# Kernel tuning notes

Hardware: AMD Instinct MI355X
Metric: run time of the kernel (lower is better)

## Reference

```python
import jax, jax.numpy as jnp
import numpy as np

T, B, F, H, L = 512, 64, 128, 512, 3
SCALES = [1, 2, 4]  # 2**l for l in range(n_layers)


def setup_inputs() -> dict:
    key = jax.random.key(0)
    ks = jax.random.split(key, 10)
    s = 0.05
    inp = {"inputs": jax.random.normal(ks[0], (B, T, F), jnp.float32)}
    in_dims = [F, H, H]
    i = 1
    for l in range(L):
        inp[f"wi{l}"] = jax.random.normal(ks[i], (in_dims[l], H), jnp.float32) * s; i += 1
        inp[f"ws{l}"] = jax.random.normal(ks[i], (F, H), jnp.float32) * s; i += 1
        inp[f"wh{l}"] = jax.random.normal(ks[i], (H, H), jnp.float32) * s; i += 1
    return inp


def _scaled(x, scale):
    # x: [T, B, F]; moving average over time with window `scale`, stride 1
    if scale == 1:
        return x
    cs = jnp.concatenate([jnp.zeros((1,) + x.shape[1:], x.dtype), jnp.cumsum(x, axis=0)], axis=0)
    return (cs[scale:] - cs[:-scale]) / scale  # [T-scale+1, B, F]


def _layer(inp, sx, wi, ws, wh, scale):
    # loop i in range(len(sx) - scale), index = scale-1+i; hidden starts at zeros
    n = sx.shape[0] - scale
    xs = inp[scale - 1:scale - 1 + n]   # [n, B, din]
    sxs = sx[scale - 1:scale - 1 + n]   # [n, B, F]
    h0 = jnp.zeros((inp.shape[1], wh.shape[0]), inp.dtype)

    def step(h, xt):
        x_t, s_t = xt
        h = jnp.tanh(x_t @ wi + h @ wh + s_t @ ws)
        return h, h

    _, out = jax.lax.scan(step, h0, (xs, sxs))
    return out  # [n, B, H]


def reference(inputs, wi0, ws0, wh0, wi1, ws1, wh1, wi2, ws2, wh2):
    x = jnp.transpose(inputs, (1, 0, 2))  # batch_first -> [T, B, F]
    weights = [(wi0, ws0, wh0), (wi1, ws1, wh1), (wi2, ws2, wh2)]
    outs = []
    cur = x
    for l, scale in enumerate(SCALES):
        sx = _scaled(x, scale)  # scaled input always from original sequence
        cur = _layer(cur, sx, *weights[l], scale)
        outs.append(cur)
    return tuple(outs)
```

## Files before the change

kernel.cpp:

```cpp
#include <hip/hip_runtime.h>

#define T_DIM 512
#define B_DIM 64
#define F_DIM 128
#define H_DIM 512

typedef _Float16 f16x8 __attribute__((ext_vector_type(8)));
typedef _Float16 f16x4 __attribute__((ext_vector_type(4)));
typedef float f32x4 __attribute__((ext_vector_type(4)));

__global__ void prepT(_Float16* __restrict__ dst, const float* __restrict__ src) {
  int idx = blockIdx.x * blockDim.x + threadIdx.x;
  if (idx < 262144) {
    int j = idx >> 9, k = idx & 511;
    dst[idx] = (_Float16)src[k * 512 + j];
  }
}

__global__ void prep_wcat2(_Float16* __restrict__ dst, const float* __restrict__ wi0,
                           const float* __restrict__ ws0, const float* __restrict__ ws1,
                           const float* __restrict__ ws2) {
  const long total = 3L * 512 * 640;
  for (long idx = (long)blockIdx.x * blockDim.x + threadIdx.x; idx < total;
       idx += (long)gridDim.x * blockDim.x) {
    int l = (int)(idx / 327680);
    int rem = (int)(idx % 327680);
    int n = rem / 640, kc = rem % 640;
    float v = 0.f;
    if (l == 0) {
      if (kc < 128) v = wi0[kc * 512 + n];
      else if (kc < 256) v = ws0[(kc - 128) * 512 + n];
    } else {
      const float* ws = (l == 1) ? ws1 : ws2;
      if (kc < 128) v = ws[kc * 512 + n];
    }
    dst[idx] = (_Float16)v;
  }
}

__global__ void build_A(_Float16* __restrict__ Abuf, const float* __restrict__ xin,
                        const float* __restrict__ prev, int n, int inK, int scale,
                        int layer) {
  const int Kcat = inK + 128;
  const long total = (long)n * 64 * Kcat;
  for (long idx = (long)blockIdx.x * blockDim.x + threadIdx.x; idx < total;
       idx += (long)gridDim.x * blockDim.x) {
    int k = (int)(idx % Kcat);
    long r = idx / Kcat;
    int b = (int)(r & 63);
    int t = (int)(r >> 6);
    float v;
    if (k < inK) {
      if (layer == 0) v = xin[((long)b * T_DIM + t) * F_DIM + k];
      else v = prev[((long)(t + scale - 1) * B_DIM + b) * H_DIM + k];
    } else {
      int kk = k - inK;
      int t0 = t + scale - 1;
      float s = 0.f;
      for (int w = 0; w < scale; ++w) s += xin[((long)b * T_DIM + t0 + w) * F_DIM + kk];
      v = s * (1.f / scale);
    }
    Abuf[idx] = (_Float16)v;
  }
}

__global__ __launch_bounds__(256) void gemm_f16(const _Float16* __restrict__ A,
                                                const _Float16* __restrict__ Bt,
                                                float* __restrict__ C, int Mrows,
                                                int Kcat) {
  __shared__ _Float16 As[128][72];
  __shared__ _Float16 Bs[128][72];
  const int tid = threadIdx.x;
  const int tn = blockIdx.x, tm = blockIdx.y;
  const int lane = tid & 63, wid = tid >> 6;
  const int wm = wid >> 1, wn = wid & 1;
  f32x4 acc[4][4] = {};
  const int nK = Kcat >> 6;
  const int lrow = tid >> 3, lkc = (tid & 7) * 8;

  for (int kt = 0; kt < nK; ++kt) {
    for (int r = 0; r < 4; ++r) {
      int row = r * 32 + lrow;
      int grow = tm * 128 + row;
      uint4 va = make_uint4(0u, 0u, 0u, 0u);
      if (grow < Mrows) va = *(const uint4*)&A[(size_t)grow * Kcat + kt * 64 + lkc];
      *(uint4*)&As[row][lkc] = va;
      uint4 vb = *(const uint4*)&Bt[(size_t)(tn * 128 + row) * 640 + kt * 64 + lkc];
      *(uint4*)&Bs[row][lkc] = vb;
    }
    __syncthreads();
#pragma unroll
    for (int kk = 0; kk < 64; kk += 32) {
      f16x8 af[4], bf[4];
#pragma unroll
      for (int mt = 0; mt < 4; ++mt)
        af[mt] = *(const f16x8*)&As[wm * 64 + mt * 16 + (lane & 15)][kk + (lane >> 4) * 8];
#pragma unroll
      for (int nt = 0; nt < 4; ++nt)
        bf[nt] = *(const f16x8*)&Bs[wn * 64 + nt * 16 + (lane & 15)][kk + (lane >> 4) * 8];
#pragma unroll
      for (int mt = 0; mt < 4; ++mt)
#pragma unroll
        for (int nt = 0; nt < 4; ++nt)
          acc[mt][nt] = __builtin_amdgcn_mfma_f32_16x16x32_f16(af[mt], bf[nt], acc[mt][nt], 0, 0, 0);
    }
    __syncthreads();
  }

  const int crow0 = tm * 128 + wm * 64 + (lane >> 4) * 4;
  const int ccol0 = tn * 128 + wn * 64 + (lane & 15);
#pragma unroll
  for (int mt = 0; mt < 4; ++mt)
#pragma unroll
    for (int q = 0; q < 4; ++q) {
      int grow = crow0 + mt * 16 + q;
      if (grow < Mrows) {
#pragma unroll
        for (int nt = 0; nt < 4; ++nt)
          C[(size_t)grow * 512 + ccol0 + nt * 16] = acc[mt][nt][q];
      }
    }
}

__global__ void zero_cnt(int* __restrict__ c, int ntot) {
  int i = blockIdx.x * blockDim.x + threadIdx.x;
  if (i < ntot) c[i] = 0;
}

__global__ __launch_bounds__(512, 2) void pipeline(
    float* __restrict__ out, const _Float16* __restrict__ whT16,
    const _Float16* __restrict__ wiT16, int* __restrict__ prog) {
  __shared__ _Float16 stageBuf[2][16 * 512];
  __shared__ _Float16 Blds[4 * 32 * 64 * 8];

  const int wg = blockIdx.x;
  const int s = wg >> 2, g = wg & 2 ? (wg & 3) : (wg & 3);
  const int gg = wg & 3;
  (void)s; (void)g;
  const int stage = wg >> 2;
  const int tid = threadIdx.x;
  const int lane = tid & 63, wid = tid >> 6;
  const int colbase = wid * 64;
  const int bq = lane & 15;
  const int u = lane >> 4;
  const int gnb = wid * 4;

  const int nL[3] = {511, 509, 505};
  const size_t offL[3] = {0, 511ul * 32768, (511ul + 509ul) * 32768};

  if ((stage == 0) || (stage == 3) || (stage == 6)) {
    const int l = stage / 3;
    const int n = nL[l];
    float* po = out + offL[l];
    const _Float16* whT = whT16 + (size_t)l * 262144;
    int* pub = (l < 2) ? prog + stage * 4 + gg : nullptr;
    const int* src = (l > 0) ? prog + (stage - 1) * 4 + gg : nullptr;
    const int b0g = gg * 16;

    {
      uint4* B4 = (uint4*)Blds;
      for (int p = 0; p < 16; ++p) {
        int flat = p * 512 + tid;
        int ll = flat & 63;
        int gn = (flat >> 6) & 31;
        int kbl = flat >> 11;
        B4[flat] = *(const uint4*)&whT[(size_t)(gn * 16 + (ll & 15)) * 512 +
                                       (kbl + 10) * 32 + (ll >> 4) * 8];
      }
    }
    f16x8 bfr[4][10];
    {
#pragma unroll
      for (int nt = 0; nt < 4; ++nt) {
        const int j = colbase + nt * 16 + bq;
#pragma unroll
        for (int kb = 0; kb < 10; ++kb)
          bfr[nt][kb] = *(const f16x8*)&whT[(size_t)j * 512 + kb * 32 + u * 8];
      }
#pragma unroll
      for (int nt = 0; nt < 4; ++nt)
#pragma unroll
        for (int kb = 0; kb < 10; ++kb) asm volatile("" : "+v"(bfr[nt][kb]));
    }
    __syncthreads();

    const size_t base = (size_t)(b0g + bq) * 512 + colbase + u * 4;

#define AFRD(kb) (*(const f16x8*)&hs[((kb)*64 + u * 16 + (bq ^ (u & 1))) * 8])
#define BLRD(kb, nt) \
  (*(const f16x8*)&Blds[((((kb)-10) * 32 + gnb + (nt)) * 64 + lane) * 8])
#define GLOAD(kb, nt) \
  (*(const f16x8*)&whT[(size_t)(colbase + (nt)*16 + bq) * 512 + (kb)*32 + u * 8])

    for (int t = 0; t < n; ++t) {
      if (src && (t & 7) == 0) {
        if (tid == 0) {
          int target = t + 8 < n ? t + 8 : n;
          long it = 0;
          while (__hip_atomic_load(src, __ATOMIC_ACQUIRE, __HIP_MEMORY_SCOPE_AGENT) < target)
            if (++it > 100000000L) break;
        }
        __syncthreads();
        __threadfence();
      }

      const float* pc = po + (size_t)t * 32768 + base;
      f32x4 pre[4];
#pragma unroll
      for (int nt = 0; nt < 4; ++nt) pre[nt] = *(const f32x4*)&pc[nt * 16];

      f32x4 acc[4] = {};
      if (t > 0) {
        const _Float16* hs = stageBuf[(t - 1) & 1];
        constexpr int seq[16] = {10, 0, 1, 2, 3, 11, 4, 5, 14, 12, 6, 7, 13, 8, 9, 15};
        constexpr int lnx[16] = {11, -1, -1, -1, -1, 12, -1, -1, -1, 13, -1, -1, -1, -1, -1, -1};
        f16x8 afr[4];
#pragma unroll
        for (int i = 0; i < 4; ++i) afr[i] = AFRD(seq[i]);
        f16x8 blr[4];
#pragma unroll
        for (int nt = 0; nt < 4; ++nt) blr[nt] = BLRD(10, nt);
        f16x8 gfr[4];
#pragma unroll
        for (int nt = 0; nt < 4; ++nt) gfr[nt] = GLOAD(14, nt);

#pragma unroll
        for (int i = 0; i < 16; ++i) {
          const int kb = seq[i];
          f16x8 a = afr[i & 3];
          if (i + 4 < 16) afr[i & 3] = AFRD(seq[i + 4]);
          if (kb < 10) {
#pragma unroll
            for (int nt = 0; nt < 4; ++nt)
              acc[nt] = __builtin_amdgcn_mfma_f32_16x16x32_f16(bfr[nt][kb], a, acc[nt], 0, 0, 0);
          } else if (kb < 14) {
            f16x8 w[4];
#pragma unroll
            for (int nt = 0; nt < 4; ++nt) w[nt] = blr[nt];
            if (lnx[i] >= 0) {
#pragma unroll
              for (int nt = 0; nt < 4; ++nt) blr[nt] = BLRD(lnx[i], nt);
            }
#pragma unroll
            for (int nt = 0; nt < 4; ++nt)
              acc[nt] = __builtin_amdgcn_mfma_f32_16x16x32_f16(w[nt], a, acc[nt], 0, 0, 0);
          } else if (kb == 14) {
            f16x8 w[4];
#pragma unroll
            for (int nt = 0; nt < 4; ++nt) w[nt] = gfr[nt];
#pragma unroll
            for (int nt = 0; nt < 4; ++nt) gfr[nt] = GLOAD(15, nt);
#pragma unroll
            for (int nt = 0; nt < 4; ++nt)
              acc[nt] = __builtin_amdgcn_mfma_f32_16x16x32_f16(w[nt], a, acc[nt], 0, 0, 0);
          } else {
#pragma unroll
            for (int nt = 0; nt < 4; ++nt)
              acc[nt] = __builtin_amdgcn_mfma_f32_16x16x32_f16(gfr[nt], a, acc[nt], 0, 0, 0);
          }
        }
      }

      _Float16* hw = stageBuf[t & 1];
      float* pw = po + (size_t)t * 32768 + base;
#pragma unroll
      for (int nt = 0; nt < 4; ++nt) {
        const int J = colbase + nt * 16 + u * 4;
        const int slot = (J >> 5) * 64 + ((J >> 3) & 3) * 16 + (bq ^ ((J >> 3) & 1));
        f16x4 h4;
#pragma unroll
        for (int q = 0; q < 4; ++q) {
          float a = acc[nt][q] + pre[nt][q];
          float e = __builtin_amdgcn_exp2f(a * 2.8853900817779268f);
          float h = 1.f - 2.f * __builtin_amdgcn_rcpf(e + 1.f);
          acc[nt][q] = h;
          h4[q] = (_Float16)h;
        }
        *(f16x4*)&hw[slot * 8 + (J & 7)] = h4;
        *(f32x4*)&pw[nt * 16] = acc[nt];
      }

      if (pub && (((t & 7) == 7) || (t == n - 1))) {
        asm volatile("s_waitcnt vmcnt(0) lgkmcnt(0)\n\ts_barrier" ::: "memory");
        __threadfence();
        if (tid == 0)
          __hip_atomic_store(pub, t + 1, __ATOMIC_RELEASE, __HIP_MEMORY_SCOPE_AGENT);
      } else {
        asm volatile("s_waitcnt lgkmcnt(0)\n\ts_barrier" ::: "memory");
      }
    }
#undef AFRD
#undef BLRD
#undef GLOAD
  } else {
    const int l = (stage <= 2) ? 1 : 2;
    const int ha = (stage == 2 || stage == 5) ? 1 : 0;
    const int n = nL[l], nprev = nL[l - 1];
    const int off = (l == 1) ? 1 : 3;
    const float* xsrc = out + offL[l - 1];
    float* pdst = out + offL[l];
    const _Float16* wiT = wiT16 + (size_t)(l - 1) * 262144;
    int* pub = prog + stage * 4 + gg;
    const int* srcX = prog + ((l == 1) ? 0 : 3) * 4 + gg;
    const int* srcA = ha ? (prog + (stage - 1) * 4 + gg) : nullptr;

    f16x8 bfr8[4][8];
    {
#pragma unroll
      for (int nt = 0; nt < 4; ++nt) {
        const int j = colbase + nt * 16 + bq;
#pragma unroll
        for (int kb = 0; kb < 8; ++kb)
          bfr8[nt][kb] = *(const f16x8*)&wiT[(size_t)j * 512 + (ha * 8 + kb) * 32 + u * 8];
      }
#pragma unroll
      for (int nt = 0; nt < 4; ++nt)
#pragma unroll
        for (int kb = 0; kb < 8; ++kb) asm volatile("" : "+v"(bfr8[nt][kb]));
    }

    const int bx = tid & 15;
    const int jbi = tid >> 4;
    const int slotW = (jbi >> 2) * 64 + (jbi & 3) * 16 + (bx ^ (jbi & 1));
    const size_t xrowbase = (size_t)(gg * 16 + bx) * 512 + ha * 256 + jbi * 8;
    const size_t base = (size_t)(gg * 16 + bq) * 512 + colbase + u * 4;

    if (tid == 0) {
      int target = 9 + off < nprev ? 9 + off : nprev;
      long it = 0;
      while (__hip_atomic_load(srcX, __ATOMIC_ACQUIRE, __HIP_MEMORY_SCOPE_AGENT) < target)
        if (++it > 100000000L) break;
      if (srcA) {
        int ta = 8 < n ? 8 : n;
        it = 0;
        while (__hip_atomic_load(srcA, __ATOMIC_ACQUIRE, __HIP_MEMORY_SCOPE_AGENT) < ta)
          if (++it > 100000000L) break;
      }
    }
    __syncthreads();
    __threadfence();
    {
      const float* xr = xsrc + (size_t)off * 32768 + xrowbase;
      float4 xa = *(const float4*)&xr[0];
      float4 xb = *(const float4*)&xr[4];
      f16x8 xh;
      xh[0] = (_Float16)xa.x; xh[1] = (_Float16)xa.y;
      xh[2] = (_Float16)xa.z; xh[3] = (_Float16)xa.w;
      xh[4] = (_Float16)xb.x; xh[5] = (_Float16)xb.y;
      xh[6] = (_Float16)xb.z; xh[7] = (_Float16)xb.w;
      *(f16x8*)&stageBuf[0][slotW * 8] = xh;
    }
    asm volatile("s_waitcnt lgkmcnt(0)\n\ts_barrier" ::: "memory");

#define AFP(kb) \
  (*(const f16x8*)&hs[((kb)*64 + u * 16 + (bq ^ (u & 1))) * 8])

    for (int t = 0; t < n; ++t) {
      if ((t & 7) == 0 && t) {
        if (tid == 0) {
          int target = t + 9 + off < nprev ? t + 9 + off : nprev;
          long it = 0;
          while (__hip_atomic_load(srcX, __ATOMIC_ACQUIRE, __HIP_MEMORY_SCOPE_AGENT) < target)
            if (++it > 100000000L) break;
          if (srcA) {
            int ta = t + 8 < n ? t + 8 : n;
            it = 0;
            while (__hip_atomic_load(srcA, __ATOMIC_ACQUIRE, __HIP_MEMORY_SCOPE_AGENT) < ta)
              if (++it > 100000000L) break;
          }
        }
        __syncthreads();
        __threadfence();
      }

      const bool havN = (t + 1 < n);
      float4 xa, xb;
      if (havN) {
        const float* xr = xsrc + (size_t)(t + 1 + off) * 32768 + xrowbase;
        xa = *(const float4*)&xr[0];
        xb = *(const float4*)&xr[4];
      }

      f32x4 acc[4] = {};
      {
        const _Float16* hs = stageBuf[t & 1];
        f16x8 afr[4];
#pragma unroll
        for (int i = 0; i < 4; ++i) afr[i] = AFP(i);
#pragma unroll
        for (int kb = 0; kb < 8; ++kb) {
          f16x8 a = afr[kb & 3];
          if (kb < 4) afr[kb & 3] = AFP(kb + 4);
#pragma unroll
          for (int nt = 0; nt < 4; ++nt)
            acc[nt] = __builtin_amdgcn_mfma_f32_16x16x32_f16(bfr8[nt][kb], a, acc[nt], 0, 0, 0);
        }
      }

      float* pw = pdst + (size_t)t * 32768 + base;
#pragma unroll
      for (int nt = 0; nt < 4; ++nt) {
        f32x4 v = *(const f32x4*)&pw[nt * 16];
        v += acc[nt];
        *(f32x4*)&pw[nt * 16] = v;
      }

      if (havN) {
        f16x8 xh;
        xh[0] = (_Float16)xa.x; xh[1] = (_Float16)xa.y;
        xh[2] = (_Float16)xa.z; xh[3] = (_Float16)xa.w;
        xh[4] = (_Float16)xb.x; xh[5] = (_Float16)xb.y;
        xh[6] = (_Float16)xb.z; xh[7] = (_Float16)xb.w;
        *(f16x8*)&stageBuf[(t + 1) & 1][slotW * 8] = xh;
      }

      if (((t & 7) == 7) || (t == n - 1)) {
        asm volatile("s_waitcnt vmcnt(0) lgkmcnt(0)\n\ts_barrier" ::: "memory");
        __threadfence();
        if (tid == 0)
          __hip_atomic_store(pub, t + 1, __ATOMIC_RELEASE, __HIP_MEMORY_SCOPE_AGENT);
      } else {
        asm volatile("s_waitcnt lgkmcnt(0)\n\ts_barrier" ::: "memory");
      }
    }
#undef AFP
  }
}

extern "C" void kernel_launch(void* const* d_in, const int* in_sizes, int n_in,
                              void* d_out, int out_size, void* d_ws, size_t ws_size,
                              hipStream_t stream) {
  const float* inputs = (const float*)d_in[0];
  const float* wi[3] = {(const float*)d_in[1], (const float*)d_in[4], (const float*)d_in[7]};
  const float* wsm[3] = {(const float*)d_in[2], (const float*)d_in[5], (const float*)d_in[8]};
  const float* wh[3] = {(const float*)d_in[3], (const float*)d_in[6], (const float*)d_in[9]};
  float* out = (float*)d_out;

  char* wsp = (char*)d_ws;
  _Float16* whT16 = (_Float16*)wsp;
  _Float16* wiT16 = (_Float16*)(wsp + 1572864);
  _Float16* wcat = (_Float16*)(wsp + 2621440);
  int* prog = (int*)(wsp + 4587520);
  _Float16* Abuf = (_Float16*)(wsp + 4587776);

  zero_cnt<<<1, 64, 0, stream>>>(prog, 24);
  for (int l = 0; l < 3; ++l)
    prepT<<<1024, 256, 0, stream>>>(whT16 + (size_t)l * 262144, wh[l]);
  prepT<<<1024, 256, 0, stream>>>(wiT16, wi[1]);
  prepT<<<1024, 256, 0, stream>>>(wiT16 + 262144, wi[2]);
  prep_wcat2<<<1024, 256, 0, stream>>>(wcat, wi[0], wsm[0], wsm[1], wsm[2]);

  const int nL[3] = {511, 509, 505};
  const long offL[3] = {0L, 511L * 32768, (511L + 509L) * 32768};

  build_A<<<4096, 256, 0, stream>>>(Abuf, inputs, nullptr, nL[0], 128, 1, 0);
  gemm_f16<<<dim3(4, (nL[0] * 64 + 127) / 128), 256, 0, stream>>>(
      Abuf, wcat, out, nL[0] * 64, 256);
  build_A<<<2048, 256, 0, stream>>>(Abuf, inputs, nullptr, nL[1], 0, 2, 1);
  gemm_f16<<<dim3(4, (nL[1] * 64 + 127) / 128), 256, 0, stream>>>(
      Abuf, wcat + 512 * 640, out + offL[1], nL[1] * 64, 128);
  build_A<<<2048, 256, 0, stream>>>(Abuf, inputs, nullptr, nL[2], 0, 4, 1);
  gemm_f16<<<dim3(4, (nL[2] * 64 + 127) / 128), 256, 0, stream>>>(
      Abuf, wcat + 2 * 512 * 640, out + offL[2], nL[2] * 64, 128);

  pipeline<<<28, 512, 0, stream>>>(out, whT16, wiT16, prog);
}
```

Measured before the change: 2.964 ms.

## Restructure pipeline into 5 stages with fp16 ring buffers between layers

Reduces the persistent pipeline from 7 stages (28 workgroups) to 5 stages (20 workgroups). Each input-projection stage now runs a full K=512 MFMA per timestep instead of two K=256 half-stages. Hidden states go between stages through 64-entry fp16 ring buffers, and input projections are passed as fp16 values to the next recurrent stage. That stage adds them before tanh, which replaces the fp32 read-modify-write of the output. Back-pressure counters with a 40-step lag keep the rings from overflowing, at the cost of extra spin-waits and fp16 rounding of the projected inputs.

New measurement: 3.239 ms. 1.09x slower.

```diff
diff --git a/kernel.cpp b/kernel.cpp
--- a/kernel.cpp
+++ b/kernel.cpp
@@ -129,15 +129,14 @@
 
 __global__ __launch_bounds__(512, 2) void pipeline(
     float* __restrict__ out, const _Float16* __restrict__ whT16,
-    const _Float16* __restrict__ wiT16, int* __restrict__ prog) {
+    const _Float16* __restrict__ wiT16, _Float16* __restrict__ h16r,
+    _Float16* __restrict__ preIr, int* __restrict__ prog) {
   __shared__ _Float16 stageBuf[2][16 * 512];
   __shared__ _Float16 Blds[4 * 32 * 64 * 8];
 
   const int wg = blockIdx.x;
-  const int s = wg >> 2, g = wg & 2 ? (wg & 3) : (wg & 3);
+  const int stage = wg >> 2;
   const int gg = wg & 3;
-  (void)s; (void)g;
-  const int stage = wg >> 2;
   const int tid = threadIdx.x;
   const int lane = tid & 63, wid = tid >> 6;
   const int colbase = wid * 64;
@@ -147,121 +146,139 @@
 
   const int nL[3] = {511, 509, 505};
   const size_t offL[3] = {0, 511ul * 32768, (511ul + 509ul) * 32768};
-
-  if ((stage == 0) || (stage == 3) || (stage == 6)) {
-    const int l = stage / 3;
-    const int n = nL[l];
-    float* po = out + offL[l];
-    const _Float16* whT = whT16 + (size_t)l * 262144;
-    int* pub = (l < 2) ? prog + stage * 4 + gg : nullptr;
-    const int* src = (l > 0) ? prog + (stage - 1) * 4 + gg : nullptr;
-    const int b0g = gg * 16;
-
-    {
-      uint4* B4 = (uint4*)Blds;
-      for (int p = 0; p < 16; ++p) {
-        int flat = p * 512 + tid;
-        int ll = flat & 63;
-        int gn = (flat >> 6) & 31;
-        int kbl = flat >> 11;
-        B4[flat] = *(const uint4*)&whT[(size_t)(gn * 16 + (ll & 15)) * 512 +
-                                       (kbl + 10) * 32 + (ll >> 4) * 8];
-      }
-    }
-    f16x8 bfr[4][10];
-    {
-#pragma unroll
-      for (int nt = 0; nt < 4; ++nt) {
-        const int j = colbase + nt * 16 + bq;
-#pragma unroll
-        for (int kb = 0; kb < 10; ++kb)
-          bfr[nt][kb] = *(const f16x8*)&whT[(size_t)j * 512 + kb * 32 + u * 8];
-      }
-#pragma unroll
-      for (int nt = 0; nt < 4; ++nt)
-#pragma unroll
-        for (int kb = 0; kb < 10; ++kb) asm volatile("" : "+v"(bfr[nt][kb]));
-    }
-    __syncthreads();
-
-    const size_t base = (size_t)(b0g + bq) * 512 + colbase + u * 4;
+  const bool isRec = (stage & 1) == 0;
+  const int l = isRec ? (stage >> 1) : ((stage + 1) >> 1);
+
+  const _Float16* W = isRec ? (whT16 + (size_t)l * 262144)
+                            : (wiT16 + (size_t)(l - 1) * 262144);
+
+  {
+    uint4* B4 = (uint4*)Blds;
+    for (int p = 0; p < 16; ++p) {
+      int flat = p * 512 + tid;
+      int ll = flat & 63;
+      int gn = (flat >> 6) & 31;
+      int kbl = flat >> 11;
+      B4[flat] = *(const uint4*)&W[(size_t)(gn * 16 + (ll & 15)) * 512 +
+                                   (kbl + 10) * 32 + (ll >> 4) * 8];
+    }
+  }
+  f16x8 bfr[4][10];
+  {
+#pragma unroll
+    for (int nt = 0; nt < 4; ++nt) {
+      const int j = colbase + nt * 16 + bq;
+#pragma unroll
+      for (int kb = 0; kb < 10; ++kb)
+        bfr[nt][kb] = *(const f16x8*)&W[(size_t)j * 512 + kb * 32 + u * 8];
+    }
+#pragma unroll
+    for (int nt = 0; nt < 4; ++nt)
+#pragma unroll
+      for (int kb = 0; kb < 10; ++kb) asm volatile("" : "+v"(bfr[nt][kb]));
+  }
+  __syncthreads();
 
 #define AFRD(kb) (*(const f16x8*)&hs[((kb)*64 + u * 16 + (bq ^ (u & 1))) * 8])
 #define BLRD(kb, nt) \
   (*(const f16x8*)&Blds[((((kb)-10) * 32 + gnb + (nt)) * 64 + lane) * 8])
 #define GLOAD(kb, nt) \
-  (*(const f16x8*)&whT[(size_t)(colbase + (nt)*16 + bq) * 512 + (kb)*32 + u * 8])
+  (*(const f16x8*)&W[(size_t)(colbase + (nt)*16 + bq) * 512 + (kb)*32 + u * 8])
+
+#define MFMA16()                                                                 \
+  {                                                                              \
+    constexpr int seq[16] = {10, 0, 1, 2, 3, 11, 4, 5, 14, 12, 6, 7, 13, 8, 9, 15}; \
+    constexpr int lnx[16] = {11, -1, -1, -1, -1, 12, -1, -1, -1, 13, -1, -1, -1, -1, -1, -1}; \
+    f16x8 afr[4];                                                                \
+    _Pragma("unroll") for (int i = 0; i < 4; ++i) afr[i] = AFRD(seq[i]);         \
+    f16x8 blr[4];                                                                \
+    _Pragma("unroll") for (int nt = 0; nt < 4; ++nt) blr[nt] = BLRD(10, nt);     \
+    f16x8 gfr[4];                                                                \
+    _Pragma("unroll") for (int nt = 0; nt < 4; ++nt) gfr[nt] = GLOAD(14, nt);    \
+    _Pragma("unroll") for (int i = 0; i < 16; ++i) {                             \
+      const int kb = seq[i];                                                     \
+      f16x8 a = afr[i & 3];                                                      \
+      if (i + 4 < 16) afr[i & 3] = AFRD(seq[i + 4]);                             \
+      if (kb < 10) {                                                             \
+        _Pragma("unroll") for (int nt = 0; nt < 4; ++nt)                         \
+            acc[nt] = __builtin_amdgcn_mfma_f32_16x16x32_f16(bfr[nt][kb], a,     \
+                                                             acc[nt], 0, 0, 0); \
+      } else if (kb < 14) {                                                      \
+        f16x8 w[4];                                                              \
+        _Pragma("unroll") for (int nt = 0; nt < 4; ++nt) w[nt] = blr[nt];        \
+        if (lnx[i] >= 0) {                                                       \
+          _Pragma("unroll") for (int nt = 0; nt < 4; ++nt) blr[nt] =             \
+              BLRD(lnx[i], nt);                                                  \
+        }                                                                        \
+        _Pragma("unroll") for (int nt = 0; nt < 4; ++nt)                         \
+            acc[nt] = __builtin_amdgcn_mfma_f32_16x16x32_f16(w[nt], a, acc[nt],  \
+                                                             0, 0, 0);          \
+      } else if (kb == 14) {                                                     \
+        f16x8 w[4];                                                              \
+        _Pragma("unroll") for (int nt = 0; nt < 4; ++nt) w[nt] = gfr[nt];        \
+        _Pragma("unroll") for (int nt = 0; nt < 4; ++nt) gfr[nt] = GLOAD(15, nt);\
+        _Pragma("unroll") for (int nt = 0; nt < 4; ++nt)                         \
+            acc[nt] = __builtin_amdgcn_mfma_f32_16x16x32_f16(w[nt], a, acc[nt],  \
+                                                             0, 0, 0);          \
+      } else {                                                                   \
+        _Pragma("unroll") for (int nt = 0; nt < 4; ++nt)                         \
+            acc[nt] = __builtin_amdgcn_mfma_f32_16x16x32_f16(gfr[nt], a,         \
+                                                             acc[nt], 0, 0, 0); \
+      }                                                                          \
+    }                                                                            \
+  }
+
+  if (isRec) {
+    const int n = nL[l];
+    float* po = out + offL[l];
+    int* pub = prog + stage * 4 + gg;
+    const int* fwd = (l > 0) ? prog + (stage - 1) * 4 + gg : nullptr;
+    const int* bpc = (l < 2) ? prog + (stage + 1) * 4 + gg : nullptr;
+    const _Float16* preIrd =
+        (l > 0) ? preIr + ((size_t)(l - 1) * 4 + gg) * 524288 : nullptr;
+    _Float16* h16w = (l < 2) ? h16r + ((size_t)l * 4 + gg) * 524288 : nullptr;
+    const int b0g = gg * 16;
+    const size_t base = (size_t)(b0g + bq) * 512 + colbase + u * 4;
+    const int riOff = bq * 512 + colbase + u * 4;
 
     for (int t = 0; t < n; ++t) {
-      if (src && (t & 7) == 0) {
+      if ((t & 7) == 0) {
         if (tid == 0) {
-          int target = t + 8 < n ? t + 8 : n;
           long it = 0;
-          while (__hip_atomic_load(src, __ATOMIC_ACQUIRE, __HIP_MEMORY_SCOPE_AGENT) < target)
-            if (++it > 100000000L) break;
+          if (fwd) {
+            int tgt = t + 8 < n ? t + 8 : n;
+            while (__hip_atomic_load(fwd, __ATOMIC_ACQUIRE, __HIP_MEMORY_SCOPE_AGENT) < tgt)
+              if (++it > 200000000L) break;
+          }
+          if (bpc && t > 40) {
+            it = 0;
+            while (__hip_atomic_load(bpc, __ATOMIC_ACQUIRE, __HIP_MEMORY_SCOPE_AGENT) < t - 40)
+              if (++it > 200000000L) break;
+          }
         }
         __syncthreads();
         __threadfence();
       }
 
       const float* pc = po + (size_t)t * 32768 + base;
-      f32x4 pre[4];
-#pragma unroll
-      for (int nt = 0; nt < 4; ++nt) pre[nt] = *(const f32x4*)&pc[nt * 16];
+      f32x4 preS[4];
+#pragma unroll
+      for (int nt = 0; nt < 4; ++nt) preS[nt] = *(const f32x4*)&pc[nt * 16];
+      f16x4 pi4[4];
+      if (preIrd) {
+        const _Float16* ps = preIrd + (size_t)(t & 63) * 8192 + riOff;
+#pragma unroll
+        for (int nt = 0; nt < 4; ++nt) pi4[nt] = *(const f16x4*)&ps[nt * 16];
+      }
 
       f32x4 acc[4] = {};
       if (t > 0) {
         const _Float16* hs = stageBuf[(t - 1) & 1];
-        constexpr int seq[16] = {10, 0, 1, 2, 3, 11, 4, 5, 14, 12, 6, 7, 13, 8, 9, 15};
-        constexpr int lnx[16] = {11, -1, -1, -1, -1, 12, -1, -1, -1, 13, -1, -1, -1, -1, -1, -1};
-        f16x8 afr[4];
-#pragma unroll
-        for (int i = 0; i < 4; ++i) afr[i] = AFRD(seq[i]);
-        f16x8 blr[4];
-#pragma unroll
-        for (int nt = 0; nt < 4; ++nt) blr[nt] = BLRD(10, nt);
-        f16x8 gfr[4];
-#pragma unroll
-        for (int nt = 0; nt < 4; ++nt) gfr[nt] = GLOAD(14, nt);
-
-#pragma unroll
-        for (int i = 0; i < 16; ++i) {
-          const int kb = seq[i];
-          f16x8 a = afr[i & 3];
-          if (i + 4 < 16) afr[i & 3] = AFRD(seq[i + 4]);
-          if (kb < 10) {
-#pragma unroll
-            for (int nt = 0; nt < 4; ++nt)
-              acc[nt] = __builtin_amdgcn_mfma_f32_16x16x32_f16(bfr[nt][kb], a, acc[nt], 0, 0, 0);
-          } else if (kb < 14) {
-            f16x8 w[4];
-#pragma unroll
-            for (int nt = 0; nt < 4; ++nt) w[nt] = blr[nt];
-            if (lnx[i] >= 0) {
-#pragma unroll
-              for (int nt = 0; nt < 4; ++nt) blr[nt] = BLRD(lnx[i], nt);
-            }
-#pragma unroll
-            for (int nt = 0; nt < 4; ++nt)
-              acc[nt] = __builtin_amdgcn_mfma_f32_16x16x32_f16(w[nt], a, acc[nt], 0, 0, 0);
-          } else if (kb == 14) {
-            f16x8 w[4];
-#pragma unroll
-            for (int nt = 0; nt < 4; ++nt) w[nt] = gfr[nt];
-#pragma unroll
-            for (int nt = 0; nt < 4; ++nt) gfr[nt] = GLOAD(15, nt);
-#pragma unroll
-            for (int nt = 0; nt < 4; ++nt)
-              acc[nt] = __builtin_amdgcn_mfma_f32_16x16x32_f16(w[nt], a, acc[nt], 0, 0, 0);
-          } else {
-#pragma unroll
-            for (int nt = 0; nt < 4; ++nt)
-              acc[nt] = __builtin_amdgcn_mfma_f32_16x16x32_f16(gfr[nt], a, acc[nt], 0, 0, 0);
-          }
-        }
+        MFMA16();
       }
 
       _Float16* hw = stageBuf[t & 1];
+      _Float16* hrw = h16w ? h16w + (size_t)(t & 63) * 8192 : nullptr;
       float* pw = po + (size_t)t * 32768 + base;
 #pragma unroll
       for (int nt = 0; nt < 4; ++nt) {
@@ -270,148 +287,16 @@
         f16x4 h4;
 #pragma unroll
         for (int q = 0; q < 4; ++q) {
-          float a = acc[nt][q] + pre[nt][q];
+          float a = acc[nt][q] + preS[nt][q];
+          if (preIrd) a += (float)pi4[nt][q];
           float e = __builtin_amdgcn_exp2f(a * 2.8853900817779268f);
           float h = 1.f - 2.f * __builtin_amdgcn_rcpf(e + 1.f);
           acc[nt][q] = h;
           h4[q] = (_Float16)h;
         }
         *(f16x4*)&hw[slot * 8 + (J & 7)] = h4;
+        if (hrw) *(f16x4*)&hrw[slot * 8 + (J & 7)] = h4;
         *(f32x4*)&pw[nt * 16] = acc[nt];
-      }
-
-      if (pub && (((t & 7) == 7) || (t == n - 1))) {
-        asm volatile("s_waitcnt vmcnt(0) lgkmcnt(0)\n\ts_barrier" ::: "memory");
-        __threadfence();
-        if (tid == 0)
-          __hip_atomic_store(pub, t + 1, __ATOMIC_RELEASE, __HIP_MEMORY_SCOPE_AGENT);
-      } else {
-        asm volatile("s_waitcnt lgkmcnt(0)\n\ts_barrier" ::: "memory");
-      }
-    }
-#undef AFRD
-#undef BLRD
-#undef GLOAD
-  } else {
-    const int l = (stage <= 2) ? 1 : 2;
-    const int ha = (stage == 2 || stage == 5) ? 1 : 0;
-    const int n = nL[l], nprev = nL[l - 1];
-    const int off = (l == 1) ? 1 : 3;
-    const float* xsrc = out + offL[l - 1];
-    float* pdst = out + offL[l];
-    const _Float16* wiT = wiT16 + (size_t)(l - 1) * 262144;
-    int* pub = prog + stage * 4 + gg;
-    const int* srcX = prog + ((l == 1) ? 0 : 3) * 4 + gg;
-    const int* srcA = ha ? (prog + (stage - 1) * 4 + gg) : nullptr;
-
-    f16x8 bfr8[4][8];
-    {
-#pragma unroll
-      for (int nt = 0; nt < 4; ++nt) {
-        const int j = colbase + nt * 16 + bq;
-#pragma unroll
-        for (int kb = 0; kb < 8; ++kb)
-          bfr8[nt][kb] = *(const f16x8*)&wiT[(size_t)j * 512 + (ha * 8 + kb) * 32 + u * 8];
-      }
-#pragma unroll
-      for (int nt = 0; nt < 4; ++nt)
-#pragma unroll
-        for (int kb = 0; kb < 8; ++kb) asm volatile("" : "+v"(bfr8[nt][kb]));
-    }
-
-    const int bx = tid & 15;
-    const int jbi = tid >> 4;
-    const int slotW = (jbi >> 2) * 64 + (jbi & 3) * 16 + (bx ^ (jbi & 1));
-    const size_t xrowbase = (size_t)(gg * 16 + bx) * 512 + ha * 256 + jbi * 8;
-    const size_t base = (size_t)(gg * 16 + bq) * 512 + colbase + u * 4;
-
-    if (tid == 0) {
-      int target = 9 + off < nprev ? 9 + off : nprev;
-      long it = 0;
-      while (__hip_atomic_load(srcX, __ATOMIC_ACQUIRE, __HIP_MEMORY_SCOPE_AGENT) < target)
-        if (++it > 100000000L) break;
-      if (srcA) {
-        int ta = 8 < n ? 8 : n;
-        it = 0;
-        while (__hip_atomic_load(srcA, __ATOMIC_ACQUIRE, __HIP_MEMORY_SCOPE_AGENT) < ta)
-          if (++it > 100000000L) break;
-      }
-    }
-    __syncthreads();
-    __threadfence();
-    {
-      const float* xr = xsrc + (size_t)off * 32768 + xrowbase;
-      float4 xa = *(const float4*)&xr[0];
-      float4 xb = *(const float4*)&xr[4];
-      f16x8 xh;
-      xh[0] = (_Float16)xa.x; xh[1] = (_Float16)xa.y;
-      xh[2] = (_Float16)xa.z; xh[3] = (_Float16)xa.w;
-      xh[4] = (_Float16)xb.x; xh[5] = (_Float16)xb.y;
-      xh[6] = (_Float16)xb.z; xh[7] = (_Float16)xb.w;
-      *(f16x8*)&stageBuf[0][slotW * 8] = xh;
-    }
-    asm volatile("s_waitcnt lgkmcnt(0)\n\ts_barrier" ::: "memory");
-
-#define AFP(kb) \
-  (*(const f16x8*)&hs[((kb)*64 + u * 16 + (bq ^ (u & 1))) * 8])
-
-    for (int t = 0; t < n; ++t) {
-      if ((t & 7) == 0 && t) {
-        if (tid == 0) {
-          int target = t + 9 + off < nprev ? t + 9 + off : nprev;
-          long it = 0;
-          while (__hip_atomic_load(srcX, __ATOMIC_ACQUIRE, __HIP_MEMORY_SCOPE_AGENT) < target)
-            if (++it > 100000000L) break;
-          if (srcA) {
-            int ta = t + 8 < n ? t + 8 : n;
-            it = 0;
-            while (__hip_atomic_load(srcA, __ATOMIC_ACQUIRE, __HIP_MEMORY_SCOPE_AGENT) < ta)
-              if (++it > 100000000L) break;
-          }
-        }
-        __syncthreads();
-        __threadfence();
-      }
-
-      const bool havN = (t + 1 < n);
-      float4 xa, xb;
-      if (havN) {
-        const float* xr = xsrc + (size_t)(t + 1 + off) * 32768 + xrowbase;
-        xa = *(const float4*)&xr[0];
-        xb = *(const float4*)&xr[4];
-      }
-
-      f32x4 acc[4] = {};
-      {
-        const _Float16* hs = stageBuf[t & 1];
-        f16x8 afr[4];
-#pragma unroll
-        for (int i = 0; i < 4; ++i) afr[i] = AFP(i);
-#pragma unroll
-        for (int kb = 0; kb < 8; ++kb) {
-          f16x8 a = afr[kb & 3];
-          if (kb < 4) afr[kb & 3] = AFP(kb + 4);
-#pragma unroll
-          for (int nt = 0; nt < 4; ++nt)
-            acc[nt] = __builtin_amdgcn_mfma_f32_16x16x32_f16(bfr8[nt][kb], a, acc[nt], 0, 0, 0);
-        }
-      }
-
-      float* pw = pdst + (size_t)t * 32768 + base;
-#pragma unroll
-      for (int nt = 0; nt < 4; ++nt) {
-        f32x4 v = *(const f32x4*)&pw[nt * 16];
-        v += acc[nt];
-        *(f32x4*)&pw[nt * 16] = v;
-      }
-
-      if (havN) {
-        f16x8 xh;
-        xh[0] = (_Float16)xa.x; xh[1] = (_Float16)xa.y;
-        xh[2] = (_Float16)xa.z; xh[3] = (_Float16)xa.w;
-        xh[4] = (_Float16)xb.x; xh[5] = (_Float16)xb.y;
-        xh[6] = (_Float16)xb.z; xh[7] = (_Float16)xb.w;
-        *(f16x8*)&stageBuf[(t + 1) & 1][slotW * 8] = xh;
       }
 
       if (((t & 7) == 7) || (t == n - 1)) {
@@ -423,8 +308,90 @@
         asm volatile("s_waitcnt lgkmcnt(0)\n\ts_barrier" ::: "memory");
       }
     }
-#undef AFP
-  }
+  } else {
+    const int n = nL[l], nprev = nL[l - 1];
+    const int off = (l == 1) ? 1 : 3;
+    int* pub = prog + stage * 4 + gg;
+    const int* fwd = prog + (stage - 1) * 4 + gg;
+    const int* bpc = prog + (stage + 1) * 4 + gg;
+    const _Float16* h16rd = h16r + ((size_t)(l - 1) * 4 + gg) * 524288;
+    _Float16* preIw = preIr + ((size_t)(l - 1) * 4 + gg) * 524288;
+    const int riOff = bq * 512 + colbase + u * 4;
+
+    if (tid == 0) {
+      int tgt = 9 + off < nprev ? 9 + off : nprev;
+      long it = 0;
+      while (__hip_atomic_load(fwd, __ATOMIC_ACQUIRE, __HIP_MEMORY_SCOPE_AGENT) < tgt)
+        if (++it > 200000000L) break;
+    }
+    __syncthreads();
+    __threadfence();
+    {
+      const uint4* rs = (const uint4*)(h16rd + (size_t)(off & 63) * 8192);
+      ((uint4*)stageBuf[0])[2 * tid] = rs[2 * tid];
+      ((uint4*)stageBuf[0])[2 * tid + 1] = rs[2 * tid + 1];
+    }
+    asm volatile("s_waitcnt lgkmcnt(0)\n\ts_barrier" ::: "memory");
+
+    for (int t = 0; t < n; ++t) {
+      if ((t & 7) == 0 && t) {
+        if (tid == 0) {
+          long it = 0;
+          int tgt = t + 9 + off < nprev ? t + 9 + off : nprev;
+          while (__hip_atomic_load(fwd, __ATOMIC_ACQUIRE, __HIP_MEMORY_SCOPE_AGENT) < tgt)
+            if (++it > 200000000L) break;
+          if (t > 40) {
+            it = 0;
+            while (__hip_atomic_load(bpc, __ATOMIC_ACQUIRE, __HIP_MEMORY_SCOPE_AGENT) < t - 40)
+              if (++it > 200000000L) break;
+          }
+        }
+        __syncthreads();
+        __threadfence();
+      }
+
+      const bool havN = (t + 1 < n);
+      uint4 xa, xb;
+      if (havN) {
+        const uint4* rs = (const uint4*)(h16rd + (size_t)((t + 1 + off) & 63) * 8192);
+        xa = rs[2 * tid];
+        xb = rs[2 * tid + 1];
+      }
+
+      f32x4 acc[4] = {};
+      {
+        const _Float16* hs = stageBuf[t & 1];
+        MFMA16();
+      }
+
+      _Float16* pwr = preIw + (size_t)(t & 63) * 8192 + riOff;
+#pragma unroll
+      for (int nt = 0; nt < 4; ++nt) {
+        f16x4 v;
+#pragma unroll
+        for (int q = 0; q < 4; ++q) v[q] = (_Float16)acc[nt][q];
+        *(f16x4*)&pwr[nt * 16] = v;
+      }
+
+      if (havN) {
+        ((uint4*)stageBuf[(t + 1) & 1])[2 * tid] = xa;
+        ((uint4*)stageBuf[(t + 1) & 1])[2 * tid + 1] = xb;
+      }
+
+      if (((t & 7) == 7) || (t == n - 1)) {
+        asm volatile("s_waitcnt vmcnt(0) lgkmcnt(0)\n\ts_barrier" ::: "memory");
+        __threadfence();
+        if (tid == 0)
+          __hip_atomic_store(pub, t + 1, __ATOMIC_RELEASE, __HIP_MEMORY_SCOPE_AGENT);
+      } else {
+        asm volatile("s_waitcnt lgkmcnt(0)\n\ts_barrier" ::: "memory");
+      }
+    }
+  }
+#undef AFRD
+#undef BLRD
+#undef GLOAD
+#undef MFMA16
 }
 
 extern "C" void kernel_launch(void* const* d_in, const int* in_sizes, int n_in,
@@ -441,9 +408,11 @@
   _Float16* wiT16 = (_Float16*)(wsp + 1572864);
   _Float16* wcat = (_Float16*)(wsp + 2621440);
   int* prog = (int*)(wsp + 4587520);
+  _Float16* h16r = (_Float16*)(wsp + 4587776);
+  _Float16* preIr = (_Float16*)(wsp + 4587776 + 8388608);
   _Float16* Abuf = (_Float16*)(wsp + 4587776);
 
-  zero_cnt<<<1, 64, 0, stream>>>(prog, 24);
+  zero_cnt<<<1, 64, 0, stream>>>(prog, 32);
   for (int l = 0; l < 3; ++l)
     prepT<<<1024, 256, 0, stream>>>(whT16 + (size_t)l * 262144, wh[l]);
   prepT<<<1024, 256, 0, stream>>>(wiT16, wi[1]);
@@ -463,5 +432,5 @@
   gemm_f16<<<dim3(4, (nL[2] * 64 + 127) / 128), 256, 0, stream>>>(
       Abuf, wcat + 2 * 512 * 640, out + offL[2], nL[2] * 64, 128);
 
-  pipeline<<<28, 512, 0, stream>>>(out, whT16, wiT16, prog);
-}
+  pipeline<<<20, 512, 0, stream>>>(out, whT16, wiT16, h16r, preIr, prog);
+}
```
